# Kernel tuning notes

Hardware: AMD Instinct MI355X
Metric: run time of the kernel (lower is better)

## Reference

```python
import jax, jax.numpy as jnp
import numpy as np

H_LSTM = 100
FORGET_BIAS = 1.0  # TF LSTMCell default


def conv2d(x, w, b, relu=True):
    # x: [N,H,W,Cin], w: [kh,kw,Cin,Cout]
    y = jax.lax.conv_general_dilated(
        x, w, window_strides=(1, 1), padding='SAME',
        dimension_numbers=('NHWC', 'HWIO', 'NHWC')) + b
    return jax.nn.relu(y) if relu else y


def lstm(xs, W, b):
    # xs: [T, N, D]; W: [D+H, 4H] with TF gate order (i, j, f, o); b: [4H]
    N = xs.shape[1]
    H = W.shape[1] // 4
    c0 = jnp.zeros((N, H), xs.dtype)
    h0 = jnp.zeros((N, H), xs.dtype)

    def step(carry, x_t):
        c, h = carry
        z = jnp.concatenate([x_t, h], axis=-1) @ W + b
        i, j, f, o = jnp.split(z, 4, axis=-1)
        c = jax.nn.sigmoid(f + FORGET_BIAS) * c + jax.nn.sigmoid(i) * jnp.tanh(j)
        h = jax.nn.sigmoid(o) * jnp.tanh(c)
        return (c, h), h

    _, hs = jax.lax.scan(step, (c0, h0), xs)
    return hs  # [T, N, H]


def setup_inputs() -> dict:
    B, L, C = 64, 55, 24
    key = jax.random.key(0)
    ks = jax.random.split(key, 32)
    s = 0.05
    inp = {'x': jax.random.normal(ks[0], (B, 13, 13, L, C), jnp.float32)}
    # 1x1 conv block (p1)
    cins = [C, 30, 30, 30]
    for i in range(4):
        inp[f'w1{i}'] = jax.random.normal(ks[1 + i], (1, 1, cins[i], 30), jnp.float32) * s
        inp[f'b1{i}'] = jnp.zeros((30,), jnp.float32)
    # 5x5 conv block (p2)
    for i in range(4):
        inp[f'w2{i}'] = jax.random.normal(ks[5 + i], (5, 5, 30, 30), jnp.float32) * s
        inp[f'b2{i}'] = jnp.zeros((30,), jnp.float32)
    # LSTM layers: inputs 30 -> 100 and 100 -> 100
    inp['lstm1_w'] = jax.random.uniform(ks[9], (30 + H_LSTM, 4 * H_LSTM), jnp.float32, -0.1, 0.1)
    inp['lstm1_b'] = jnp.zeros((4 * H_LSTM,), jnp.float32)
    inp['lstm2_w'] = jax.random.uniform(ks[10], (H_LSTM + H_LSTM, 4 * H_LSTM), jnp.float32, -0.1, 0.1)
    inp['lstm2_b'] = jnp.zeros((4 * H_LSTM,), jnp.float32)
    # final 1x1 conv, no activation
    inp['we'] = jax.random.normal(ks[11], (1, 1, H_LSTM, 1), jnp.float32) * s
    inp['be'] = jnp.zeros((1,), jnp.float32)
    return inp


def reference(x, w10, b10, w11, b11, w12, b12, w13, b13,
              w20, b20, w21, b21, w22, b22, w23, b23,
              lstm1_w, lstm1_b, lstm2_w, lstm2_b, we, be):
    B, _, _, L, C = x.shape
    # [B,13,13,L,C] -> [L,B,13,13,C] -> [L*B,13,13,C]
    h = jnp.transpose(x, (3, 0, 1, 2, 4)).reshape(L * B, 13, 13, C)
    for w, b in ((w10, b10), (w11, b11), (w12, b12), (w13, b13),
                 (w20, b20), (w21, b21), (w22, b22), (w23, b23)):
        h = conv2d(h, w, b, relu=True)
    # time-major sequence: [L, B*13*13, 30]
    h = h.reshape(L, B * 13 * 13, 30)
    h = lstm(h, lstm1_w, lstm1_b)
    h = lstm(h, lstm2_w, lstm2_b)
    h = h.reshape(L * B, 13, 13, H_LSTM)
    h = conv2d(h, we, be, relu=False)  # [L*B,13,13,1]
    h = h.reshape(L, B, 13, 13)
    return jnp.transpose(h, (1, 2, 3, 0))  # [B,13,13,L]
```

## Files before the change

### kernel.cpp

```cpp
#include <hip/hip_runtime.h>
#include <math.h>

#define N_ROWS 10816
#define T_SEQ 55
#define NPIX 169

__device__ __forceinline__ unsigned short f2bf(float f){
    unsigned u = __float_as_uint(f);
    unsigned r = u + 0x7FFFu + ((u>>16)&1u);
    return (unsigned short)(r>>16);
}
__device__ __forceinline__ float bf2f(unsigned short h){
    return __uint_as_float(((unsigned)h)<<16);
}

__device__ __forceinline__ float fast_rcp(float x){
    return __builtin_amdgcn_rcpf(x);
}
__device__ __forceinline__ float fast_sig(float x){
    return fast_rcp(1.0f + __expf(-x));
}
__device__ __forceinline__ float fast_tanh(float x){
    float ax = fabsf(x);
    float e  = __expf(-2.0f*ax);
    float r  = (1.0f - e)*fast_rcp(1.0f + e);
    return copysignf(r, x);
}

typedef __attribute__((ext_vector_type(8))) short bfrag;
typedef __attribute__((ext_vector_type(8))) _Float16 hfrag;
typedef __attribute__((ext_vector_type(4))) float facc;

__global__ __launch_bounds__(256) void conv1x1_chain(
    const float* __restrict__ x,
    const float* __restrict__ w0, const float* __restrict__ b0,
    const float* __restrict__ w1, const float* __restrict__ b1,
    const float* __restrict__ w2, const float* __restrict__ b2,
    const float* __restrict__ w3, const float* __restrict__ b3,
    float* __restrict__ out)
{
    int n = blockIdx.x*256 + threadIdx.x;
    int l = blockIdx.y;
    if (n >= N_ROWS) return;
    const float* xp = x + ((size_t)n*T_SEQ + l)*24;
    float in24[24];
    #pragma unroll
    for (int i=0;i<6;i++){
        float4 v = *(const float4*)(xp + 4*i);
        in24[4*i]=v.x; in24[4*i+1]=v.y; in24[4*i+2]=v.z; in24[4*i+3]=v.w;
    }
    float a[30], c[30];
    #pragma unroll
    for (int co=0;co<30;co++) a[co]=b0[co];
    #pragma unroll
    for (int ci=0;ci<24;ci++){
        float v = in24[ci];
        #pragma unroll
        for (int co=0;co<30;co++) a[co] = fmaf(v, w0[ci*30+co], a[co]);
    }
    #pragma unroll
    for (int co=0;co<30;co++) a[co] = fmaxf(a[co],0.f);

#define LAYER30(wp, bp) \
    { _Pragma("unroll") for (int co=0;co<30;co++) c[co]=(bp)[co]; \
      _Pragma("unroll") for (int ci=0;ci<30;ci++){ float v=a[ci]; \
        _Pragma("unroll") for (int co=0;co<30;co++) c[co]=fmaf(v,(wp)[ci*30+co],c[co]); } \
      _Pragma("unroll") for (int co=0;co<30;co++) a[co]=fmaxf(c[co],0.f); }

    LAYER30(w1,b1);
    LAYER30(w2,b2);
    LAYER30(w3,b3);
#undef LAYER30

    float* op = out + (size_t)l*30*N_ROWS + n;
    #pragma unroll
    for (int co=0;co<30;co++) op[(size_t)co*N_ROWS] = a[co];
}

__global__ __launch_bounds__(256) void repack_conv(
    const float* __restrict__ w20, const float* __restrict__ w21,
    const float* __restrict__ w22, const float* __restrict__ w23,
    unsigned short* __restrict__ cwh, unsigned short* __restrict__ cwl)
{
    int i = blockIdx.x*256 + threadIdx.x;
    if (i >= 4*25600) return;
    int layer = i / 25600, r = i - layer*25600;
    int frag = r >> 9, e = r & 511;
    int kt = frag >> 1, ct = frag & 1;
    int lane = e >> 3, j = e & 7;
    int ci = ((lane>>4)<<3) + j;
    int co = ct*16 + (lane & 15);
    const float* w = (layer==0)?w20:(layer==1)?w21:(layer==2)?w22:w23;
    float v = (ci<30 && co<30) ? w[(size_t)(kt*30 + ci)*30 + co] : 0.f;
    unsigned short h = f2bf(v);
    cwh[i] = h; cwl[i] = f2bf(v - bf2f(h));
}

__global__ __launch_bounds__(256, 4) void conv5x5_mfma4(
    float* __restrict__ buf,
    const unsigned short* __restrict__ cwh, const unsigned short* __restrict__ cwl,
    const float* __restrict__ bias0, const float* __restrict__ bias1,
    const float* __restrict__ bias2, const float* __restrict__ bias3)
{
    __shared__ __align__(16) unsigned short imgh[18*17*32];
    __shared__ __align__(16) unsigned short imgl[18*17*32];

    int bi = blockIdx.x;
    int l = bi >> 6, b = bi & 63;
    float* ip = buf + (size_t)l*30*N_ROWS + (size_t)b*NPIX;
    const int tid = threadIdx.x;
    const int wave = tid >> 6, lane = tid & 63;
    const int m16 = lane & 15, quad = lane >> 4;

    {
        unsigned* zh = (unsigned*)imgh; unsigned* zl = (unsigned*)imgl;
        for (int i=tid; i<18*17*16; i+=256){ zh[i]=0u; zl[i]=0u; }
    }
    __syncthreads();

    for (int i=tid; i<30*NPIX; i+=256){
        int ci = i / NPIX, p = i - ci*NPIX;
        int py = p/13, px = p - py*13;
        float v = ip[(size_t)ci*N_ROWS + p];
        int L = (py+2)*17 + (px+2);
        int o = L*32 + ((((ci>>3) + L)&3)<<3) + (ci&7);
        unsigned short hh = f2bf(v);
        imgh[o] = hh; imgl[o] = f2bf(v - bf2f(hh));
    }

    int pL[3]; bool mv[3];
    #pragma unroll
    for (int mi=0; mi<3; mi++){
        int Mt = wave + mi*4;
        mv[mi] = (Mt < 11);
        int p = Mt*16 + m16;
        int py = p/13, px = p - py*13;
        pL[mi] = py*17 + px;
    }

    #pragma unroll 1
    for (int layer=0; layer<4; layer++){
        const float* bias = (layer==0)?bias0:(layer==1)?bias1:(layer==2)?bias2:bias3;
        const unsigned short* wh = cwh + (size_t)layer*25600;
        const unsigned short* wl = cwl + (size_t)layer*25600;

        __syncthreads();

        float bb[2];
        #pragma unroll
        for (int nt=0; nt<2; nt++){
            int co = nt*16 + m16;
            bb[nt] = (co < 30) ? bias[co] : 0.f;
        }
        facc acc[3][2];
        #pragma unroll
        for (int mi=0; mi<3; mi++)
            #pragma unroll
            for (int nt=0; nt<2; nt++)
                acc[mi][nt] = (facc){bb[nt], bb[nt], bb[nt], bb[nt]};

        #pragma unroll 1
        for (int kt=0; kt<25; kt++){
            int dy = kt/5, dx = kt - dy*5;
            int Ld = dy*17 + dx;
            bfrag ah[3], al[3];
            #pragma unroll
            for (int mi=0; mi<3; mi++){
                if (mv[mi]){
                    int L = pL[mi] + Ld;
                    int o = L*32 + (((quad + L)&3)<<3);
                    ah[mi] = *(const bfrag*)(imgh + o);
                    al[mi] = *(const bfrag*)(imgl + o);
                }
            }
            const unsigned short* whp = wh + (size_t)(kt*2)*512 + lane*8;
            const unsigned short* wlp = wl + (size_t)(kt*2)*512 + lane*8;
            bfrag bh0 = *(const bfrag*)(whp);
            bfrag bh1 = *(const bfrag*)(whp + 512);
            bfrag bl0 = *(const bfrag*)(wlp);
            bfrag bl1 = *(const bfrag*)(wlp + 512);
            #pragma unroll
            for (int mi=0; mi<3; mi++){
                if (mv[mi]){
                    acc[mi][0] = __builtin_amdgcn_mfma_f32_16x16x32_bf16(ah[mi], bh0, acc[mi][0],0,0,0);
                    acc[mi][1] = __builtin_amdgcn_mfma_f32_16x16x32_bf16(ah[mi], bh1, acc[mi][1],0,0,0);
                }
            }
            #pragma unroll
            for (int mi=0; mi<3; mi++){
                if (mv[mi]){
                    acc[mi][0] = __builtin_amdgcn_mfma_f32_16x16x32_bf16(al[mi], bh0, acc[mi][0],0,0,0);
                    acc[mi][1] = __builtin_amdgcn_mfma_f32_16x16x32_bf16(al[mi], bh1, acc[mi][1],0,0,0);
                }
            }
            #pragma unroll
            for (int mi=0; mi<3; mi++){
                if (mv[mi]){
                    acc[mi][0] = __builtin_amdgcn_mfma_f32_16x16x32_bf16(ah[mi], bl0, acc[mi][0],0,0,0);
                    acc[mi][1] = __builtin_amdgcn_mfma_f32_16x16x32_bf16(ah[mi], bl1, acc[mi][1],0,0,0);
                }
            }
        }

        __syncthreads();

        if (layer < 3){
            #pragma unroll
            for (int mi=0; mi<3; mi++){
                if (mv[mi]){
                    int Mt = wave + mi*4;
                    #pragma unroll
                    for (int nt=0; nt<2; nt++){
                        int co = nt*16 + m16;
                        if (co < 30){
                            #pragma unroll
                            for (int i2=0; i2<4; i2++){
                                int p = Mt*16 + quad*4 + i2;
                                if (p < NPIX){
                                    float v = fmaxf(acc[mi][nt][i2], 0.f);
                                    int py = p/13, px = p - py*13;
                                    int L = (py+2)*17 + (px+2);
                                    int o = L*32 + ((((co>>3) + L)&3)<<3) + (co&7);
                                    unsigned short hh = f2bf(v);
                                    imgh[o] = hh; imgl[o] = f2bf(v - bf2f(hh));
                                }
                            }
                        }
                    }
                }
            }
        } else {
            #pragma unroll
            for (int mi=0; mi<3; mi++){
                if (mv[mi]){
                    int Mt = wave + mi*4;
                    #pragma unroll
                    for (int nt=0; nt<2; nt++){
                        int co = nt*16 + m16;
                        if (co < 30){
                            #pragma unroll
                            for (int i2=0; i2<4; i2++){
                                int p = Mt*16 + quad*4 + i2;
                                if (p < NPIX)
                                    ip[(size_t)co*N_ROWS + p] = fmaxf(acc[mi][nt][i2], 0.f);
                            }
                        }
                    }
                }
            }
        }
    }
}

__global__ __launch_bounds__(256) void repack_mfma_f16(
    const float* __restrict__ l1w, const float* __restrict__ l1b,
    const float* __restrict__ l2w, const float* __restrict__ l2b,
    _Float16* __restrict__ bw1, _Float16* __restrict__ bw2,
    float* __restrict__ pbias1, float* __restrict__ pbias2)
{
    const int S1 = 5*32*512;
    const int S2 = 7*32*512;
    int i = blockIdx.x*256 + threadIdx.x;
    if (i < S1){
        int fr = i >> 9, r = i & 511;
        int kt = fr >> 5, ct = fr & 31;
        int lane = r >> 3, j = r & 7;
        int k = kt*32 + ((lane>>4)<<3) + j;
        int n = lane & 15;
        int cell = ((ct>>2)<<4) + n, g = ct & 3;
        float w = (k<130 && cell<100) ? l1w[(size_t)k*400 + g*100 + cell] : 0.f;
        bw1[i] = (_Float16)w;
    } else if (i < S1 + S2){
        int ii = i - S1;
        int fr = ii >> 9, r = ii & 511;
        int kt = fr >> 5, ct = fr & 31;
        int lane = r >> 3, j = r & 7;
        int k = kt*32 + ((lane>>4)<<3) + j;
        int n = lane & 15;
        int cell = ((ct>>2)<<4) + n, g = ct & 3;
        float w = (k<200 && cell<100) ? l2w[(size_t)k*400 + g*100 + cell] : 0.f;
        bw2[ii] = (_Float16)w;
    } else if (i < S1+S2+512){
        int col = i - S1 - S2;
        int ct = col >> 4, n = col & 15;
        int cell = ((ct>>2)<<4) + n, g = ct & 3;
        pbias1[col] = (cell<100) ? l1b[g*100+cell] : 0.f;
    } else if (i < S1+S2+1024){
        int col = i - S1 - S2 - 512;
        int ct = col >> 4, n = col & 15;
        int cell = ((ct>>2)<<4) + n, g = ct & 3;
        pbias2[col] = (cell<100) ? l2b[g*100+cell] : 0.f;
    }
}

#define NKT1 5
#define NKT2 7
#define M_BLK 32
#define RSTR 40
#define KTSTR (32*RSTR)
__global__ __launch_bounds__(512, 4) void lstm_mfma11(
    const float* __restrict__ xall,
    const _Float16* __restrict__ bw1, const _Float16* __restrict__ bw2,
    const float* __restrict__ pbias1, const float* __restrict__ pbias2,
    const float* __restrict__ we, const float* __restrict__ be,
    float* __restrict__ out)
{
    __shared__ __align__(16) _Float16 A1[NKT1*KTSTR];
    __shared__ __align__(16) _Float16 A2[NKT2*KTSTR];
    __shared__ float pbuf[8*M_BLK];

    const int tid  = threadIdx.x;
    const int w    = tid >> 6, lane = tid & 63;
    const int m16  = lane & 15, quad = lane >> 4;
    const int n0   = blockIdx.x * M_BLK;
    const int cell = w*16 + m16;
    const bool cv  = (cell < 100);

    for (int i=tid; i<NKT1*KTSTR; i+=512) A1[i]=(_Float16)0.f;
    for (int i=tid; i<NKT2*KTSTR; i+=512) A2[i]=(_Float16)0.f;
    for (int i=tid; i<8*M_BLK; i+=512) pbuf[i]=0.f;

    float cs1[2][4] = {{0,0,0,0},{0,0,0,0}};
    float cs2[2][4] = {{0,0,0,0},{0,0,0,0}};
    float b1[4], b2[4];
    #pragma unroll
    for (int g=0; g<4; g++){
        b1[g] = pbias1[(w*4+g)*16 + m16];
        b2[g] = pbias2[(w*4+g)*16 + m16];
    }
    const float weC = cv ? we[cell] : 0.f;
    const float be0 = be[0];

    const _Float16* w1p = bw1 + ((size_t)(w*4)*64 + lane)*8;
    const _Float16* w2p = bw2 + ((size_t)(w*4)*64 + lane)*8;

    const int sk = tid >> 3, sq = tid & 7;

    __syncthreads();

    if (tid < 240){
        float4 v = *(const float4*)(xall + (size_t)sk*N_ROWS + n0 + sq*4);
        A1[(sq*4+0)*RSTR + sk] = (_Float16)v.x;
        A1[(sq*4+1)*RSTR + sk] = (_Float16)v.y;
        A1[(sq*4+2)*RSTR + sk] = (_Float16)v.z;
        A1[(sq*4+3)*RSTR + sk] = (_Float16)v.w;
    }
    __syncthreads();

    facc acc[2][4];

#define GEMM(W0, NKT, AH, BI) \
    { _Pragma("unroll") \
      for (int mt=0; mt<2; mt++) \
        _Pragma("unroll") \
        for (int g=0; g<4; g++){ float bb=(BI)[g]; acc[mt][g]=(facc){bb,bb,bb,bb}; } \
      _Pragma("unroll 1") \
      for (int kt=0; kt<(NKT); kt++){ \
        hfrag ah[2]; \
        _Pragma("unroll") \
        for (int mt=0; mt<2; mt++){ \
            int off = kt*KTSTR + (mt*16+m16)*RSTR + (quad<<3); \
            ah[mt] = *(const hfrag*)((AH) + off); } \
        const _Float16* whp = (W0) + (size_t)kt*16384; \
        hfrag wh[4]; \
        _Pragma("unroll") \
        for (int g=0; g<4; g++) wh[g] = *(const hfrag*)(whp + (size_t)g*512); \
        _Pragma("unroll") \
        for (int g=0; g<4; g++){ \
            acc[0][g]=__builtin_amdgcn_mfma_f32_16x16x32_f16(ah[0],wh[g],acc[0][g],0,0,0); \
            acc[1][g]=__builtin_amdgcn_mfma_f32_16x16x32_f16(ah[1],wh[g],acc[1][g],0,0,0); } \
      } }

    for (int t=0; t<T_SEQ; t++){
        float4 xn;
        if (t+1 < T_SEQ && tid < 240)
            xn = *(const float4*)(xall + ((size_t)(t+1)*30+sk)*N_ROWS + n0 + sq*4);

        GEMM(w1p, NKT1, A1, b1);
        __syncthreads();

        if (cv){
            #pragma unroll
            for (int mt=0; mt<2; mt++){
                #pragma unroll
                for (int i2=0;i2<4;i2++){
                    float gi = fast_sig(acc[mt][0][i2]);
                    float gj = fast_tanh(acc[mt][1][i2]);
                    float gf = fast_sig(acc[mt][2][i2] + 1.0f);
                    float go = fast_sig(acc[mt][3][i2]);
                    float cn = gf*cs1[mt][i2] + gi*gj;
                    cs1[mt][i2] = cn;
                    float h = go*fast_tanh(cn);
                    int row = mt*16 + quad*4 + i2;
                    _Float16 hh = (_Float16)h;
                    int k1 = 30 + cell;
                    A1[(k1>>5)*KTSTR + row*RSTR + (k1&31)] = hh;
                    A2[(cell>>5)*KTSTR + row*RSTR + (cell&31)] = hh;
                }
            }
        }
        if (t+1 < T_SEQ && tid < 240){
            A1[(sq*4+0)*RSTR + sk] = (_Float16)xn.x;
            A1[(sq*4+1)*RSTR + sk] = (_Float16)xn.y;
            A1[(sq*4+2)*RSTR + sk] = (_Float16)xn.z;
            A1[(sq*4+3)*RSTR + sk] = (_Float16)xn.w;
        }
        __syncthreads();

        GEMM(w2p, NKT2, A2, b2);
        __syncthreads();

        if (w < 7){
            float pp[2][4] = {{0,0,0,0},{0,0,0,0}};
            if (cv){
                #pragma unroll
                for (int mt=0; mt<2; mt++){
                    #pragma unroll
                    for (int i2=0;i2<4;i2++){
                        float gi = fast_sig(acc[mt][0][i2]);
                        float gj = fast_tanh(acc[mt][1][i2]);
                        float gf = fast_sig(acc[mt][2][i2] + 1.0f);
                        float go = fast_sig(acc[mt][3][i2]);
                        float cn = gf*cs2[mt][i2] + gi*gj;
                        cs2[mt][i2] = cn;
                        float h = go*fast_tanh(cn);
                        pp[mt][i2] = h*weC;
                        int row = mt*16 + quad*4 + i2;
                        int k1 = 100 + cell;
                        A2[(k1>>5)*KTSTR + row*RSTR + (k1&31)] = (_Float16)h;
                    }
                }
            }
            #pragma unroll
            for (int mt=0; mt<2; mt++){
                #pragma unroll
                for (int i2=0;i2<4;i2++){
                    float p = pp[mt][i2];
                    p += __shfl_xor(p, 1);
                    p += __shfl_xor(p, 2);
                    p += __shfl_xor(p, 4);
                    p += __shfl_xor(p, 8);
                    pp[mt][i2] = p;
                }
            }
            if (m16 == 0){
                #pragma unroll
                for (int mt=0; mt<2; mt++)
                    #pragma unroll
                    for (int i2=0;i2<4;i2++)
                        pbuf[w*M_BLK + mt*16 + quad*4 + i2] = pp[mt][i2];
            }
        }
        __syncthreads();

        if (tid < M_BLK){
            float s = be0;
            #pragma unroll
            for (int ww=0; ww<8; ww++) s += pbuf[ww*M_BLK + tid];
            out[(size_t)(n0+tid)*T_SEQ + t] = s;
        }
    }
#undef GEMM
}

extern "C" void kernel_launch(void* const* d_in, const int* in_sizes, int n_in,
                              void* d_out, int out_size, void* d_ws, size_t ws_size,
                              hipStream_t stream)
{
    const float* x    = (const float*)d_in[0];
    const float* w10  = (const float*)d_in[1];  const float* b10 = (const float*)d_in[2];
    const float* w11  = (const float*)d_in[3];  const float* b11 = (const float*)d_in[4];
    const float* w12  = (const float*)d_in[5];  const float* b12 = (const float*)d_in[6];
    const float* w13  = (const float*)d_in[7];  const float* b13 = (const float*)d_in[8];
    const float* w20  = (const float*)d_in[9];  const float* b20 = (const float*)d_in[10];
    const float* w21  = (const float*)d_in[11]; const float* b21 = (const float*)d_in[12];
    const float* w22  = (const float*)d_in[13]; const float* b22 = (const float*)d_in[14];
    const float* w23  = (const float*)d_in[15]; const float* b23 = (const float*)d_in[16];
    const float* l1w  = (const float*)d_in[17]; const float* l1b = (const float*)d_in[18];
    const float* l2w  = (const float*)d_in[19]; const float* l2b = (const float*)d_in[20];
    const float* we   = (const float*)d_in[21]; const float* be  = (const float*)d_in[22];
    float* out = (float*)d_out;

    const size_t NF = (size_t)30*N_ROWS;
    float* buf0 = (float*)d_ws;
    unsigned short* packbase = (unsigned short*)(buf0 + (size_t)T_SEQ*NF);
    _Float16* bw1 = (_Float16*)packbase;
    _Float16* bw2 = (_Float16*)(packbase + 2*(5*32*512));
    float* pbias1 = (float*)(packbase + 2*(5*32*512) + 2*(7*32*512));
    float* pbias2 = pbias1 + 512;

    unsigned short* cwh = packbase;
    unsigned short* cwl = cwh + 4*25600;

    repack_conv<<<(4*25600+255)/256, 256, 0, stream>>>(w20, w21, w22, w23, cwh, cwl);

    dim3 g1((N_ROWS+255)/256, T_SEQ);
    conv1x1_chain<<<g1, 256, 0, stream>>>(x, w10,b10, w11,b11, w12,b12, w13,b13, buf0);

    conv5x5_mfma4<<<T_SEQ*64, 256, 0, stream>>>(buf0, cwh, cwl, b20, b21, b22, b23);

    const int REPACK_N = 5*32*512 + 7*32*512 + 1024;
    repack_mfma_f16<<<(REPACK_N+255)/256, 256, 0, stream>>>(
        l1w, l1b, l2w, l2b, bw1, bw2, pbias1, pbias2);

    lstm_mfma11<<<N_ROWS/M_BLK, 512, 0, stream>>>(buf0, bw1, bw2,
                                                  pbias1, pbias2, we, be, out);
}
```

Measured before the change: 1.025 ms.

## Fuse 1x1 conv chain into 5x5 conv kernel and use single-pass fp16 MFMA

Moves the four-layer 1x1 conv chain into the 5x5 conv kernel, so each block computes its own image's 1x1 outputs straight into shared memory and no longer round-trips them through global memory. It also replaces the three-pass bf16 hi/lo split MFMA scheme with one fp16 MFMA pass, which cuts MFMA work and LDS traffic by about two thirds. In exchange, the 1x1 chain now runs on only 169 of 256 threads per block, and fp16 is less precise than the split-bf16 emulation, which risks accuracy loss or overflow.

```diff
diff --git a/kernel.cpp b/kernel.cpp
--- a/kernel.cpp
+++ b/kernel.cpp
@@ -4,15 +4,6 @@
 #define N_ROWS 10816
 #define T_SEQ 55
 #define NPIX 169
-
-__device__ __forceinline__ unsigned short f2bf(float f){
-    unsigned u = __float_as_uint(f);
-    unsigned r = u + 0x7FFFu + ((u>>16)&1u);
-    return (unsigned short)(r>>16);
-}
-__device__ __forceinline__ float bf2f(unsigned short h){
-    return __uint_as_float(((unsigned)h)<<16);
-}
 
 __device__ __forceinline__ float fast_rcp(float x){
     return __builtin_amdgcn_rcpf(x);
@@ -27,60 +18,13 @@
     return copysignf(r, x);
 }
 
-typedef __attribute__((ext_vector_type(8))) short bfrag;
 typedef __attribute__((ext_vector_type(8))) _Float16 hfrag;
 typedef __attribute__((ext_vector_type(4))) float facc;
 
-__global__ __launch_bounds__(256) void conv1x1_chain(
-    const float* __restrict__ x,
-    const float* __restrict__ w0, const float* __restrict__ b0,
-    const float* __restrict__ w1, const float* __restrict__ b1,
-    const float* __restrict__ w2, const float* __restrict__ b2,
-    const float* __restrict__ w3, const float* __restrict__ b3,
-    float* __restrict__ out)
-{
-    int n = blockIdx.x*256 + threadIdx.x;
-    int l = blockIdx.y;
-    if (n >= N_ROWS) return;
-    const float* xp = x + ((size_t)n*T_SEQ + l)*24;
-    float in24[24];
-    #pragma unroll
-    for (int i=0;i<6;i++){
-        float4 v = *(const float4*)(xp + 4*i);
-        in24[4*i]=v.x; in24[4*i+1]=v.y; in24[4*i+2]=v.z; in24[4*i+3]=v.w;
-    }
-    float a[30], c[30];
-    #pragma unroll
-    for (int co=0;co<30;co++) a[co]=b0[co];
-    #pragma unroll
-    for (int ci=0;ci<24;ci++){
-        float v = in24[ci];
-        #pragma unroll
-        for (int co=0;co<30;co++) a[co] = fmaf(v, w0[ci*30+co], a[co]);
-    }
-    #pragma unroll
-    for (int co=0;co<30;co++) a[co] = fmaxf(a[co],0.f);
-
-#define LAYER30(wp, bp) \
-    { _Pragma("unroll") for (int co=0;co<30;co++) c[co]=(bp)[co]; \
-      _Pragma("unroll") for (int ci=0;ci<30;ci++){ float v=a[ci]; \
-        _Pragma("unroll") for (int co=0;co<30;co++) c[co]=fmaf(v,(wp)[ci*30+co],c[co]); } \
-      _Pragma("unroll") for (int co=0;co<30;co++) a[co]=fmaxf(c[co],0.f); }
-
-    LAYER30(w1,b1);
-    LAYER30(w2,b2);
-    LAYER30(w3,b3);
-#undef LAYER30
-
-    float* op = out + (size_t)l*30*N_ROWS + n;
-    #pragma unroll
-    for (int co=0;co<30;co++) op[(size_t)co*N_ROWS] = a[co];
-}
-
-__global__ __launch_bounds__(256) void repack_conv(
+__global__ __launch_bounds__(256) void repack_conv_f16(
     const float* __restrict__ w20, const float* __restrict__ w21,
     const float* __restrict__ w22, const float* __restrict__ w23,
-    unsigned short* __restrict__ cwh, unsigned short* __restrict__ cwl)
+    _Float16* __restrict__ cw)
 {
     int i = blockIdx.x*256 + threadIdx.x;
     if (i >= 4*25600) return;
@@ -92,18 +36,21 @@
     int co = ct*16 + (lane & 15);
     const float* w = (layer==0)?w20:(layer==1)?w21:(layer==2)?w22:w23;
     float v = (ci<30 && co<30) ? w[(size_t)(kt*30 + ci)*30 + co] : 0.f;
-    unsigned short h = f2bf(v);
-    cwh[i] = h; cwl[i] = f2bf(v - bf2f(h));
-}
-
-__global__ __launch_bounds__(256, 4) void conv5x5_mfma4(
-    float* __restrict__ buf,
-    const unsigned short* __restrict__ cwh, const unsigned short* __restrict__ cwl,
-    const float* __restrict__ bias0, const float* __restrict__ bias1,
-    const float* __restrict__ bias2, const float* __restrict__ bias3)
+    cw[i] = (_Float16)v;
+}
+
+__global__ __launch_bounds__(256, 4) void conv_fused(
+    const float* __restrict__ x,
+    const float* __restrict__ w0, const float* __restrict__ b0,
+    const float* __restrict__ w1, const float* __restrict__ b1,
+    const float* __restrict__ w2, const float* __restrict__ b2,
+    const float* __restrict__ w3, const float* __restrict__ b3,
+    const _Float16* __restrict__ cw,
+    const float* __restrict__ cb0, const float* __restrict__ cb1,
+    const float* __restrict__ cb2, const float* __restrict__ cb3,
+    float* __restrict__ buf)
 {
-    __shared__ __align__(16) unsigned short imgh[18*17*32];
-    __shared__ __align__(16) unsigned short imgl[18*17*32];
+    __shared__ __align__(16) _Float16 img[18*17*32];
 
     int bi = blockIdx.x;
     int l = bi >> 6, b = bi & 63;
@@ -112,20 +59,45 @@
     const int wave = tid >> 6, lane = tid & 63;
     const int m16 = lane & 15, quad = lane >> 4;
 
-    {
-        unsigned* zh = (unsigned*)imgh; unsigned* zl = (unsigned*)imgl;
-        for (int i=tid; i<18*17*16; i+=256){ zh[i]=0u; zl[i]=0u; }
-    }
+    for (int i=tid; i<18*17*16; i+=256) ((unsigned*)img)[i] = 0u;
     __syncthreads();
 
-    for (int i=tid; i<30*NPIX; i+=256){
-        int ci = i / NPIX, p = i - ci*NPIX;
-        int py = p/13, px = p - py*13;
-        float v = ip[(size_t)ci*N_ROWS + p];
+    if (tid < NPIX){
+        const float* xp = x + ((size_t)(b*NPIX + tid)*T_SEQ + l)*24;
+        float in24[24];
+        #pragma unroll
+        for (int i=0;i<6;i++){
+            float4 v = *(const float4*)(xp + 4*i);
+            in24[4*i]=v.x; in24[4*i+1]=v.y; in24[4*i+2]=v.z; in24[4*i+3]=v.w;
+        }
+        float a[30], c[30];
+        #pragma unroll
+        for (int co=0;co<30;co++) a[co]=b0[co];
+        #pragma unroll
+        for (int ci=0;ci<24;ci++){
+            float v = in24[ci];
+            #pragma unroll
+            for (int co=0;co<30;co++) a[co] = fmaf(v, w0[ci*30+co], a[co]);
+        }
+        #pragma unroll
+        for (int co=0;co<30;co++) a[co] = fmaxf(a[co],0.f);
+
+#define LAYER30(wp, bp) \
+        { _Pragma("unroll") for (int co=0;co<30;co++) c[co]=(bp)[co]; \
+          _Pragma("unroll") for (int ci=0;ci<30;ci++){ float v=a[ci]; \
+            _Pragma("unroll") for (int co=0;co<30;co++) c[co]=fmaf(v,(wp)[ci*30+co],c[co]); } \
+          _Pragma("unroll") for (int co=0;co<30;co++) a[co]=fmaxf(c[co],0.f); }
+
+        LAYER30(w1,b1);
+        LAYER30(w2,b2);
+        LAYER30(w3,b3);
+#undef LAYER30
+
+        int py = tid/13, px = tid - py*13;
         int L = (py+2)*17 + (px+2);
-        int o = L*32 + ((((ci>>3) + L)&3)<<3) + (ci&7);
-        unsigned short hh = f2bf(v);
-        imgh[o] = hh; imgl[o] = f2bf(v - bf2f(hh));
+        #pragma unroll
+        for (int ci=0;ci<30;ci++)
+            img[L*32 + ((((ci>>3) + L)&3)<<3) + (ci&7)] = (_Float16)a[ci];
     }
 
     int pL[3]; bool mv[3];
@@ -140,9 +112,8 @@
 
     #pragma unroll 1
     for (int layer=0; layer<4; layer++){
-        const float* bias = (layer==0)?bias0:(layer==1)?bias1:(layer==2)?bias2:bias3;
-        const unsigned short* wh = cwh + (size_t)layer*25600;
-        const unsigned short* wl = cwl + (size_t)layer*25600;
+        const float* bias = (layer==0)?cb0:(layer==1)?cb1:(layer==2)?cb2:cb3;
+        const _Float16* wh = cw + (size_t)layer*25600;
 
         __syncthreads();
 
@@ -163,41 +134,23 @@
         for (int kt=0; kt<25; kt++){
             int dy = kt/5, dx = kt - dy*5;
             int Ld = dy*17 + dx;
-            bfrag ah[3], al[3];
+            hfrag ah[3];
             #pragma unroll
             for (int mi=0; mi<3; mi++){
                 if (mv[mi]){
                     int L = pL[mi] + Ld;
                     int o = L*32 + (((quad + L)&3)<<3);
-                    ah[mi] = *(const bfrag*)(imgh + o);
-                    al[mi] = *(const bfrag*)(imgl + o);
-                }
-            }
-            const unsigned short* whp = wh + (size_t)(kt*2)*512 + lane*8;
-            const unsigned short* wlp = wl + (size_t)(kt*2)*512 + lane*8;
-            bfrag bh0 = *(const bfrag*)(whp);
-            bfrag bh1 = *(const bfrag*)(whp + 512);
-            bfrag bl0 = *(const bfrag*)(wlp);
-            bfrag bl1 = *(const bfrag*)(wlp + 512);
+                    ah[mi] = *(const hfrag*)(img + o);
+                }
+            }
+            const _Float16* whp = wh + (size_t)(kt*2)*512 + lane*8;
+            hfrag wh0 = *(const hfrag*)(whp);
+            hfrag wh1 = *(const hfrag*)(whp + 512);
             #pragma unroll
             for (int mi=0; mi<3; mi++){
                 if (mv[mi]){
-                    acc[mi][0] = __builtin_amdgcn_mfma_f32_16x16x32_bf16(ah[mi], bh0, acc[mi][0],0,0,0);
-                    acc[mi][1] = __builtin_amdgcn_mfma_f32_16x16x32_bf16(ah[mi], bh1, acc[mi][1],0,0,0);
-                }
-            }
-            #pragma unroll
-            for (int mi=0; mi<3; mi++){
-                if (mv[mi]){
-                    acc[mi][0] = __builtin_amdgcn_mfma_f32_16x16x32_bf16(al[mi], bh0, acc[mi][0],0,0,0);
-                    acc[mi][1] = __builtin_amdgcn_mfma_f32_16x16x32_bf16(al[mi], bh1, acc[mi][1],0,0,0);
-                }
-            }
-            #pragma unroll
-            for (int mi=0; mi<3; mi++){
-                if (mv[mi]){
-                    acc[mi][0] = __builtin_amdgcn_mfma_f32_16x16x32_bf16(ah[mi], bl0, acc[mi][0],0,0,0);
-                    acc[mi][1] = __builtin_amdgcn_mfma_f32_16x16x32_bf16(ah[mi], bl1, acc[mi][1],0,0,0);
+                    acc[mi][0] = __builtin_amdgcn_mfma_f32_16x16x32_f16(ah[mi], wh0, acc[mi][0],0,0,0);
+                    acc[mi][1] = __builtin_amdgcn_mfma_f32_16x16x32_f16(ah[mi], wh1, acc[mi][1],0,0,0);
                 }
             }
         }
@@ -220,9 +173,7 @@
                                     float v = fmaxf(acc[mi][nt][i2], 0.f);
                                     int py = p/13, px = p - py*13;
                                     int L = (py+2)*17 + (px+2);
-                                    int o = L*32 + ((((co>>3) + L)&3)<<3) + (co&7);
-                                    unsigned short hh = f2bf(v);
-                                    imgh[o] = hh; imgl[o] = f2bf(v - bf2f(hh));
+                                    img[L*32 + ((((co>>3) + L)&3)<<3) + (co&7)] = (_Float16)v;
                                 }
                             }
                         }
@@ -489,15 +440,13 @@
     float* pbias1 = (float*)(packbase + 2*(5*32*512) + 2*(7*32*512));
     float* pbias2 = pbias1 + 512;
 
-    unsigned short* cwh = packbase;
-    unsigned short* cwl = cwh + 4*25600;
-
-    repack_conv<<<(4*25600+255)/256, 256, 0, stream>>>(w20, w21, w22, w23, cwh, cwl);
-
-    dim3 g1((N_ROWS+255)/256, T_SEQ);
-    conv1x1_chain<<<g1, 256, 0, stream>>>(x, w10,b10, w11,b11, w12,b12, w13,b13, buf0);
-
-    conv5x5_mfma4<<<T_SEQ*64, 256, 0, stream>>>(buf0, cwh, cwl, b20, b21, b22, b23);
+    _Float16* cwf = (_Float16*)packbase;
+
+    repack_conv_f16<<<(4*25600+255)/256, 256, 0, stream>>>(w20, w21, w22, w23, cwf);
+
+    conv_fused<<<T_SEQ*64, 256, 0, stream>>>(
+        x, w10,b10, w11,b11, w12,b12, w13,b13,
+        cwf, b20, b21, b22, b23, buf0);
 
     const int REPACK_N = 5*32*512 + 7*32*512 + 1024;
     repack_mfma_f16<<<(REPACK_N+255)/256, 256, 0, stream>>>(
```

Result: faster. 886.9 us (-13.5%).
